# Optimization experiments

Measured on AMD Instinct MI355X. Metric: run time of the kernel, lower is better.

Reference implementation:

```python
import jax, jax.numpy as jnp
import numpy as np
from jax import lax

# dims: B batch, C=d_model=256, IMG=128, P=4 patch, H=W=32, L=H*W=1024
# D=d_inner=512 (ssm_ratio 2.0), N=d_state=16, R=dt_rank=16, K=4 scan directions
B, C, IMG, P = 2, 256, 128, 4
H = W = IMG // P
L = H * W
D_INNER, N, R, K = 512, 16, 16, 4


def layernorm(x, g, b, eps=1e-5):
    mu = jnp.mean(x, axis=-1, keepdims=True)
    var = jnp.var(x, axis=-1, keepdims=True)
    return (x - mu) * lax.rsqrt(var + eps) * g + b


def setup_inputs() -> dict:
    key = jax.random.key(0)
    ks = jax.random.split(key, 12)
    f = lambda i, shape, s=0.02: jax.random.normal(ks[i], shape, jnp.float32) * s
    A_init = jnp.tile(jnp.arange(1, N + 1, dtype=jnp.float32)[None, None, :], (K, D_INNER, 1))
    return {
        "x": jax.random.normal(ks[0], (B, C, IMG, IMG), jnp.float32),
        "patch_w": f(1, (C, C, P, P)),
        "patch_b": jnp.zeros((C,), jnp.float32),
        "ln_g": jnp.ones((C,), jnp.float32),
        "ln_b": jnp.zeros((C,), jnp.float32),
        "in_w": f(2, (2 * D_INNER, C)),
        "conv_w": f(3, (D_INNER, 1, 3, 3)),
        "conv_b": jnp.zeros((D_INNER,), jnp.float32),
        "xproj_w": f(4, (K, R + 2 * N, D_INNER)),
        "dt_w": f(5, (K, D_INNER, R)),
        "dt_b": f(6, (K, D_INNER), 0.1),
        "A_log": jnp.log(A_init),
        "Ds": jnp.ones((K, D_INNER), jnp.float32),
        "on_g": jnp.ones((D_INNER,), jnp.float32),
        "on_b": jnp.zeros((D_INNER,), jnp.float32),
        "out_w": f(7, (C, D_INNER)),
        "head_w": f(8, (1, C)),
        "head_b": jnp.zeros((1,), jnp.float32),
    }


def _forward(x, patch_w, patch_b, ln_g, ln_b, in_w, conv_w, conv_b, xproj_w,
             dt_w, dt_b, A_log, Ds, on_g, on_b, out_w, head_w, head_b):
    dn = ("NCHW", "OIHW", "NCHW")
    # GRL is identity in forward. Patch embed conv, stride = patch.
    t = lax.conv_general_dilated(x, patch_w, (P, P), "VALID", dimension_numbers=dn)
    t = t + patch_b[None, :, None, None]
    t = jnp.transpose(t, (0, 2, 3, 1))                      # (B,H,W,C)

    # ---- VSS block: t + SS2D(LN(t)) ----
    u = layernorm(t, ln_g, ln_b)
    xz = jnp.einsum("bhwc,ec->bhwe", u, in_w)               # (B,H,W,2D)
    xc, z = jnp.split(xz, 2, axis=-1)
    xc = jnp.transpose(xc, (0, 3, 1, 2))                    # (B,D,H,W)
    xc = lax.conv_general_dilated(xc, conv_w, (1, 1), "SAME",
                                  dimension_numbers=dn, feature_group_count=D_INNER)
    xc = jax.nn.silu(xc + conv_b[None, :, None, None])

    # cross-scan: row-major, col-major, and their reverses -> (B,K,D,L)
    x_hw = xc.reshape(B, D_INNER, L)
    x_wh = jnp.transpose(xc, (0, 1, 3, 2)).reshape(B, D_INNER, L)
    xs = jnp.stack([x_hw, x_wh], axis=1)
    xs = jnp.concatenate([xs, jnp.flip(xs, axis=-1)], axis=1)  # (B,4,D,L)

    x_dbl = jnp.einsum("bkdl,kcd->bkcl", xs, xproj_w)          # (B,K,R+2N,L)
    dts_r = x_dbl[:, :, :R]
    Bs = x_dbl[:, :, R:R + N]                                  # (B,K,N,L)
    Cs = x_dbl[:, :, R + N:]                                   # (B,K,N,L)
    dts = jnp.einsum("bkrl,kdr->bkdl", dts_r, dt_w) + dt_b[None, :, :, None]
    dts = jax.nn.softplus(dts)                                 # (B,K,D,L)

    A = -jnp.exp(A_log)                                        # (K,D,N)
    dA = jnp.exp(dts[:, :, :, None, :] * A[None, :, :, :, None])      # (B,K,D,N,L)
    dBu = (dts * xs)[:, :, :, None, :] * Bs[:, :, None, :, :]         # (B,K,D,N,L)

    dA_t = jnp.moveaxis(dA, -1, 0)        # (L,B,K,D,N)
    dBu_t = jnp.moveaxis(dBu, -1, 0)
    Cs_t = jnp.moveaxis(Cs, -1, 0)        # (L,B,K,N)

    def step(h, inputs):
        dA_i, dBu_i, C_i = inputs
        h = dA_i * h + dBu_i
        y = jnp.einsum("bkdn,bkn->bkd", h, C_i)
        return h, y

    h0 = jnp.zeros((B, K, D_INNER, N), xs.dtype)
    _, ys = lax.scan(step, h0, (dA_t, dBu_t, Cs_t))           # ys: (L,B,K,D)
    ys = jnp.moveaxis(ys, 0, -1)                               # (B,K,D,L)
    ys = ys + Ds[None, :, :, None] * xs

    # cross-merge (invert the 4 scan orders and sum)
    y_rev = jnp.flip(ys[:, 2:], axis=-1)                        # (B,2,D,L)
    y_hw = ys[:, 0] + y_rev[:, 0]
    y_wh = ys[:, 1] + y_rev[:, 1]
    y_wh = jnp.transpose(y_wh.reshape(B, D_INNER, W, H), (0, 1, 3, 2)).reshape(B, D_INNER, L)
    y = (y_hw + y_wh).reshape(B, D_INNER, H, W)
    y = jnp.transpose(y, (0, 2, 3, 1))                          # (B,H,W,D)

    y = layernorm(y, on_g, on_b) * jax.nn.silu(z)
    ss_out = jnp.einsum("bhwd,cd->bhwc", y, out_w)
    t = t + ss_out

    # global average pool + head
    pooled = jnp.mean(t, axis=(1, 2))                           # (B,C)
    return pooled @ head_w.T + head_b


def reference(x, patch_w, patch_b, ln_g, ln_b, in_w, conv_w, conv_b, xproj_w,
              dt_w, dt_b, A_log, Ds, on_g, on_b, out_w, head_w, head_b):
    return _forward(x, patch_w, patch_b, ln_g, ln_b, in_w, conv_w, conv_b, xproj_w,
                    dt_w, dt_b, A_log, Ds, on_g, on_b, out_w, head_w, head_b)
```

## Files before the change

### kernel.cpp

```cpp
#include <hip/hip_runtime.h>
#include <math.h>


typedef __attribute__((ext_vector_type(4))) float f32x4;
typedef __attribute__((ext_vector_type(8))) short bf16x8;

__device__ __forceinline__ ushort bf16_rn(float f) {
  uint u = __float_as_uint(f);
  return (ushort)((u + 0x7fffu + ((u >> 16) & 1u)) >> 16);
}
__device__ __forceinline__ float bf2f(uint us) { return __uint_as_float(us << 16); }
__device__ __forceinline__ uint packbf(float a, float b) {
  return (uint)bf16_rn(a) | ((uint)bf16_rn(b) << 16);
}

__global__ __launch_bounds__(256) void split_all(
    const float* __restrict__ pw, const float* __restrict__ iw,
    const float* __restrict__ ow, const float* __restrict__ xw,
    ushort* __restrict__ pwh, ushort* __restrict__ pwl,
    ushort* __restrict__ iwh, ushort* __restrict__ iwl,
    ushort* __restrict__ owh, ushort* __restrict__ owl,
    ushort* __restrict__ xwh, ushort* __restrict__ xwl) {
  int i = blockIdx.x * 256 + threadIdx.x;
  const float* src; ushort* hi; ushort* lo; int off;
  if (i < 1048576)      { src = pw; hi = pwh; lo = pwl; off = i; }
  else if (i < 1310720) { src = iw; hi = iwh; lo = iwl; off = i - 1048576; }
  else if (i < 1441792) { src = ow; hi = owh; lo = owl; off = i - 1310720; }
  else if (i < 1540096) { src = xw; hi = xwh; lo = xwl; off = i - 1441792; }
  else return;
  float f = src[off];
  ushort h = bf16_rn(f);
  hi[off] = h;
  lo[off] = bf16_rn(f - __uint_as_float(((uint)h) << 16));
}

__global__ __launch_bounds__(256) void im2col_bf16(const float* __restrict__ x,
    ushort* __restrict__ Ap) {
  __shared__ __align__(16) ushort tile[32][136];
  int c0 = blockIdx.x * 8, hh = blockIdx.y, b = blockIdx.z;
  int tid = threadIdx.x;
  int ci = tid >> 5, ph = (tid >> 3) & 3, w4 = tid & 7;
  const float* src = x + (((long)(b * 256 + c0 + ci) * 128 + 4 * hh + ph) * 128 + 16 * w4);
  #pragma unroll
  for (int j = 0; j < 4; ++j) {
    float4 v = *(const float4*)(src + 4 * j);
    uint2 pk;
    pk.x = packbf(v.x, v.y);
    pk.y = packbf(v.z, v.w);
    *(uint2*)&tile[w4 * 4 + j][ci * 16 + ph * 4] = pk;
  }
  __syncthreads();
  int w = tid >> 3;
  long rowbase = ((long)(b * 1024 + hh * 32 + w)) * 4096 + c0 * 16;
  #pragma unroll
  for (int i = 0; i < 2; ++i) {
    int gr = (tid & 7) + 8 * i;
    *(uint4*)&Ap[rowbase + gr * 8] = *(const uint4*)&tile[w][gr * 8];
  }
}

__global__ __launch_bounds__(512) void mfma_bf(
    const ushort* __restrict__ A, const ushort* __restrict__ Bhi,
    const ushort* __restrict__ Blo, float* __restrict__ Cout, float* __restrict__ C2,
    int M, int N, int K, int kchunk, int mode)
{
  __shared__ __align__(16) ushort Ah[128 * 64];
  __shared__ __align__(16) ushort Bh[64 * 64];
  __shared__ __align__(16) ushort Bl[64 * 64];
  int tid = threadIdx.x;
  int n0 = blockIdx.x * 64;
  int m0 = blockIdx.y * 128;
  int k0 = blockIdx.z * kchunk;
  int wid = tid >> 6, lane = tid & 63;
  int wm = wid >> 1, wn = wid & 1;
  int lrow = lane & 15, g = lane >> 4;
  f32x4 acc[2][2] = {};
  int nkt = kchunk >> 6;
  for (int kt = 0; kt < nkt; ++kt) {
    int kb = k0 + (kt << 6);
    {
      int gi = tid & 7;
      #pragma unroll
      for (int i = 0; i < 2; ++i) {
        int row = (tid >> 3) + (i << 6);
        uint4 v = *(const uint4*)&A[(long)(m0 + row) * K + kb + gi * 8];
        *(uint4*)&Ah[row * 64 + ((gi ^ (row & 7)) << 3)] = v;
      }
      int row = tid >> 3;
      long off = (long)(n0 + row) * K + kb + gi * 8;
      int la = row * 64 + ((gi ^ (row & 7)) << 3);
      *(uint4*)&Bh[la] = *(const uint4*)&Bhi[off];
      *(uint4*)&Bl[la] = *(const uint4*)&Blo[off];
    }
    __syncthreads();
    #pragma unroll
    for (int kk = 0; kk < 2; ++kk) {
      bf16x8 af[2], bhf[2], blf[2];
      #pragma unroll
      for (int mi = 0; mi < 2; ++mi) {
        int row = wm * 32 + mi * 16 + lrow;
        af[mi] = *(const bf16x8*)&Ah[row * 64 + ((((kk << 2) + g) ^ (row & 7)) << 3)];
      }
      #pragma unroll
      for (int ni = 0; ni < 2; ++ni) {
        int row = wn * 32 + ni * 16 + lrow;
        int col = (((kk << 2) + g) ^ (row & 7)) << 3;
        bhf[ni] = *(const bf16x8*)&Bh[row * 64 + col];
        blf[ni] = *(const bf16x8*)&Bl[row * 64 + col];
      }
      #pragma unroll
      for (int mi = 0; mi < 2; ++mi)
        #pragma unroll
        for (int ni = 0; ni < 2; ++ni) {
          acc[mi][ni] = __builtin_amdgcn_mfma_f32_16x16x32_bf16(af[mi], bhf[ni], acc[mi][ni], 0, 0, 0);
          acc[mi][ni] = __builtin_amdgcn_mfma_f32_16x16x32_bf16(af[mi], blf[ni], acc[mi][ni], 0, 0, 0);
        }
    }
    __syncthreads();
  }
  int r4 = lane >> 4;
  if (mode == 2) {
    bool xhalf = (n0 < 512);
    #pragma unroll
    for (int mi = 0; mi < 2; ++mi)
      #pragma unroll
      for (int ni = 0; ni < 2; ++ni) {
        int n = n0 + wn * 32 + ni * 16 + lrow;
        int mb = m0 + wm * 32 + mi * 16 + r4 * 4;
        int bb = mb >> 10, l = mb & 1023;
        if (xhalf) {
          float4 o = make_float4(acc[mi][ni][0], acc[mi][ni][1], acc[mi][ni][2], acc[mi][ni][3]);
          *(float4*)(Cout + ((long)(bb * 512 + n)) * 1024 + l) = o;
        } else {
          #pragma unroll
          for (int r = 0; r < 4; ++r)
            C2[(long)(mb + r) * 512 + (n - 512)] = acc[mi][ni][r];
        }
      }
  } else {
    long zoff = (long)blockIdx.z * M * N;
    #pragma unroll
    for (int mi = 0; mi < 2; ++mi)
      #pragma unroll
      for (int ni = 0; ni < 2; ++ni) {
        int n = n0 + wn * 32 + ni * 16 + lrow;
        int mb = m0 + wm * 32 + mi * 16 + r4 * 4;
        #pragma unroll
        for (int r = 0; r < 4; ++r)
          Cout[zoff + (long)(mb + r) * N + n] = acc[mi][ni][r];
      }
  }
}

__global__ __launch_bounds__(256) void mfma_x(
    const ushort* __restrict__ A, const ushort* __restrict__ Bhi,
    const ushort* __restrict__ Blo, float* __restrict__ xdbl)
{
  __shared__ __align__(16) ushort Ah[64 * 64];
  __shared__ __align__(16) ushort Bh[48 * 64];
  __shared__ __align__(16) ushort Bl[48 * 64];
  int tid = threadIdx.x;
  int m0 = blockIdx.x * 64;
  int z = blockIdx.y, k = z & 3;
  const ushort* Az = A + (long)z * 524288;
  const ushort* Bhz = Bhi + (long)k * 24576;
  const ushort* Blz = Blo + (long)k * 24576;
  int lane = tid & 63, wv = tid >> 6;
  int lrow = lane & 15, g = lane >> 4;
  f32x4 acc[3] = {};
  for (int kt = 0; kt < 8; ++kt) {
    int kb = kt << 6;
    #pragma unroll
    for (int i = 0; i < 2; ++i) {
      int idx = i * 256 + tid;
      int row = idx >> 3, gi = idx & 7;
      uint4 v = *(const uint4*)&Az[(long)(m0 + row) * 512 + kb + gi * 8];
      *(uint4*)&Ah[row * 64 + ((gi ^ (row & 7)) << 3)] = v;
      if (idx < 384) {
        long off = (long)row * 512 + kb + gi * 8;
        int la = row * 64 + ((gi ^ (row & 7)) << 3);
        *(uint4*)&Bh[la] = *(const uint4*)&Bhz[off];
        *(uint4*)&Bl[la] = *(const uint4*)&Blz[off];
      }
    }
    __syncthreads();
    #pragma unroll
    for (int kk = 0; kk < 2; ++kk) {
      int arow = wv * 16 + lrow;
      bf16x8 af = *(const bf16x8*)&Ah[arow * 64 + ((((kk << 2) + g) ^ (arow & 7)) << 3)];
      #pragma unroll
      for (int ni = 0; ni < 3; ++ni) {
        int brow = ni * 16 + lrow;
        int col = (((kk << 2) + g) ^ (brow & 7)) << 3;
        bf16x8 bh = *(const bf16x8*)&Bh[brow * 64 + col];
        bf16x8 bl = *(const bf16x8*)&Bl[brow * 64 + col];
        acc[ni] = __builtin_amdgcn_mfma_f32_16x16x32_bf16(af, bh, acc[ni], 0, 0, 0);
        acc[ni] = __builtin_amdgcn_mfma_f32_16x16x32_bf16(af, bl, acc[ni], 0, 0, 0);
      }
    }
    __syncthreads();
  }
  float* Cz = xdbl + (long)z * 49152;
  int r4 = lane >> 4;
  #pragma unroll
  for (int ni = 0; ni < 3; ++ni) {
    int n = ni * 16 + lrow;
    int mb = m0 + wv * 16 + r4 * 4;
    #pragma unroll
    for (int r = 0; r < 4; ++r)
      Cz[(long)(mb + r) * 48 + n] = acc[ni][r];
  }
}

__global__ __launch_bounds__(256) void reduce_split(const float* __restrict__ P,
    float* __restrict__ C, const float* __restrict__ bias,
    int MN, int N, int S, int accumulate) {
  int i = blockIdx.x * 256 + threadIdx.x;
  if (i * 4 >= MN) return;
  float4 v = make_float4(0.f, 0.f, 0.f, 0.f);
  for (int s = 0; s < S; ++s) {
    float4 p = *(const float4*)(P + (long)s * MN + i * 4);
    v.x += p.x; v.y += p.y; v.z += p.z; v.w += p.w;
  }
  if (bias) {
    float4 bv = *(const float4*)(bias + ((i * 4) & (N - 1)));
    v.x += bv.x; v.y += bv.y; v.z += bv.z; v.w += bv.w;
  }
  if (accumulate) {
    float4 o = *(const float4*)(C + (long)i * 4);
    v.x += o.x; v.y += o.y; v.z += o.z; v.w += o.w;
  }
  *(float4*)(C + (long)i * 4) = v;
}

__device__ __forceinline__ float blk_sum(float v, float* sm) {
  #pragma unroll
  for (int o = 32; o > 0; o >>= 1) v += __shfl_down(v, o);
  int wid = threadIdx.x >> 6, lane = threadIdx.x & 63;
  __syncthreads();
  if (lane == 0) sm[wid] = v;
  __syncthreads();
  int nw = blockDim.x >> 6;
  float r = 0.f;
  for (int i = 0; i < nw; ++i) r += sm[i];
  return r;
}

__global__ __launch_bounds__(256) void reduce_ln1(const float* __restrict__ P,
    float* __restrict__ t, const float* __restrict__ bias,
    const float* __restrict__ g, const float* __restrict__ b,
    ushort* __restrict__ u) {
  __shared__ float sm[8];
  int m = blockIdx.x, c = threadIdx.x;
  float v = bias[c];
  #pragma unroll
  for (int s = 0; s < 8; ++s) v += P[(long)s * 524288 + m * 256 + c];
  t[(long)m * 256 + c] = v;
  float s1 = blk_sum(v, sm);
  float s2 = blk_sum(v * v, sm);
  float mu = s1 * (1.f / 256.f);
  float var = s2 * (1.f / 256.f) - mu * mu;
  float rs = rsqrtf(var + 1e-5f);
  u[(long)m * 256 + c] = bf16_rn((v - mu) * rs * g[c] + b[c]);
}

template<int ACT>
__global__ __launch_bounds__(256) void gemm_nt(
    const float* __restrict__ Ag, const float* __restrict__ Bg,
    const float* __restrict__ biasg, float* Cg,
    int M, int N, int Kd, int lda, int ldb, int ldc,
    long sA, long sB, long sBias, long sC, int bmod, int accumulate)
{
  __shared__ __align__(16) float As[64 * 36];
  __shared__ float Bs[32 * 33];
  int z = blockIdx.z;
  int zb = (bmod > 1) ? (z % bmod) : 0;
  const float* A = Ag + (long)z * sA;
  const float* Bm = Bg + (long)zb * sB;
  const float* bias = biasg ? (biasg + (long)zb * sBias) : nullptr;
  float* C = Cg + (long)z * sC;
  int tid = threadIdx.x;
  int n0 = blockIdx.x * 32;
  int m0 = blockIdx.y * 64;
  int tn = tid & 7, tm = tid >> 3;
  float acc[2][4] = {};
  int nk = (Kd + 31) >> 5;
  for (int kt = 0; kt < nk; ++kt) {
    int k0 = kt << 5;
    #pragma unroll
    for (int i = 0; i < 2; ++i) {
      int idx = i * 256 + tid;
      int row = idx >> 3, c4 = idx & 7;
      int m = m0 + row, k = k0 + c4 * 4;
      float4 v = make_float4(0.f, 0.f, 0.f, 0.f);
      if (m < M && k < Kd) v = *(const float4*)(A + (long)m * lda + k);
      *(float4*)&As[row * 36 + c4 * 4] = v;
    }
    {
      int row = tid >> 3, c4 = tid & 7;
      int n = n0 + row, k = k0 + c4 * 4;
      float4 v = make_float4(0.f, 0.f, 0.f, 0.f);
      if (n < N && k < Kd) v = *(const float4*)(Bm + (long)n * ldb + k);
      Bs[row * 33 + c4 * 4 + 0] = v.x;
      Bs[row * 33 + c4 * 4 + 1] = v.y;
      Bs[row * 33 + c4 * 4 + 2] = v.z;
      Bs[row * 33 + c4 * 4 + 3] = v.w;
    }
    __syncthreads();
    #pragma unroll
    for (int kk = 0; kk < 32; ++kk) {
      float a0 = As[(tm * 2 + 0) * 36 + kk];
      float a1 = As[(tm * 2 + 1) * 36 + kk];
      #pragma unroll
      for (int j = 0; j < 4; ++j) {
        float bv = Bs[(tn * 4 + j) * 33 + kk];
        acc[0][j] += a0 * bv;
        acc[1][j] += a1 * bv;
      }
    }
    __syncthreads();
  }
  bool fullN = (n0 + 32 <= N);
  #pragma unroll
  for (int i = 0; i < 2; ++i) {
    int m = m0 + tm * 2 + i;
    if (m >= M) continue;
    float r[4];
    #pragma unroll
    for (int j = 0; j < 4; ++j) {
      int n = n0 + tn * 4 + j;
      float v = acc[i][j];
      if (bias && n < N) v += bias[n];
      if (ACT == 1) v = (v > 20.f) ? v : __logf(1.f + __expf(v));
      r[j] = v;
    }
    long base = (long)m * ldc + n0 + tn * 4;
    if (fullN) {
      float4 o = make_float4(r[0], r[1], r[2], r[3]);
      if (accumulate) {
        float4 old = *(float4*)(C + base);
        o.x += old.x; o.y += old.y; o.z += old.z; o.w += old.w;
      }
      *(float4*)(C + base) = o;
    } else {
      #pragma unroll
      for (int j = 0; j < 4; ++j) {
        int n = n0 + tn * 4 + j;
        if (n < N) {
          float v = r[j];
          if (accumulate) v += C[(long)m * ldc + n];
          C[(long)m * ldc + n] = v;
        }
      }
    }
  }
}

__global__ __launch_bounds__(256) void dwconv_kernel(const float* __restrict__ xc,
    const float* __restrict__ cw, const float* __restrict__ cb, ushort* __restrict__ out) {
  __shared__ float plane[32][33];
  int d = blockIdx.x, b = blockIdx.y;
  long base = ((long)b * 512 + d) * 1024;
  int tid = threadIdx.x;
  float4 v = *(const float4*)(xc + base + tid * 4);
  int h0 = (tid * 4) >> 5, w0 = (tid * 4) & 31;
  plane[h0][w0 + 0] = v.x; plane[h0][w0 + 1] = v.y;
  plane[h0][w0 + 2] = v.z; plane[h0][w0 + 3] = v.w;
  float w9[9];
  #pragma unroll
  for (int i = 0; i < 9; ++i) w9[i] = cw[d * 9 + i];
  float bias = cb[d];
  __syncthreads();
  float o4[4];
  #pragma unroll
  for (int j = 0; j < 4; ++j) {
    int p = tid * 4 + j, h = p >> 5, w = p & 31;
    float acc = 0.f;
    #pragma unroll
    for (int dh = -1; dh <= 1; ++dh) {
      int hy = h + dh;
      if (hy < 0 || hy > 31) continue;
      #pragma unroll
      for (int dw = -1; dw <= 1; ++dw) {
        int wx = w + dw;
        if (wx < 0 || wx > 31) continue;
        acc += w9[(dh + 1) * 3 + (dw + 1)] * plane[hy][wx];
      }
    }
    acc += bias;
    o4[j] = acc / (1.f + __expf(-acc));
  }
  uint2 o2;
  o2.x = packbf(o4[0], o4[1]);
  o2.y = packbf(o4[2], o4[3]);
  *(uint2*)&out[base + tid * 4] = o2;
}

__global__ __launch_bounds__(256) void build_xsT(const ushort* __restrict__ xca,
    ushort* __restrict__ xsTb) {
  __shared__ ushort tile[32][34];
  int h = blockIdx.x;
  int d0 = blockIdx.y * 32;
  int z = blockIdx.z;
  int b = z >> 2, k = z & 3;
  int tid = threadIdx.x;
  int a = tid >> 5, q = tid & 31;
  #pragma unroll
  for (int i = 0; i < 4; ++i) {
    int di = a + i * 8;
    tile[di][q] = xca[((long)(b * 512 + d0 + di)) * 1024 + h * 32 + q];
  }
  __syncthreads();
  #pragma unroll
  for (int i = 0; i < 4; ++i) {
    int w = a + i * 8;
    int r;
    if (k == 0) r = h * 32 + w;
    else if (k == 1) r = w * 32 + h;
    else if (k == 2) r = 1023 - (h * 32 + w);
    else r = 1023 - (w * 32 + h);
    xsTb[((long)z * 1024 + r) * 512 + d0 + q] = tile[q][w];
  }
}

template<bool FINAL>
__global__ __launch_bounds__(128) void scan_chunk5(
    const float* __restrict__ dts, ushort* xsb, const float* __restrict__ xdbl,
    const float* __restrict__ A_log, const float* __restrict__ Ds,
    float* __restrict__ Pb, float* __restrict__ hpb)
{
  __shared__ float sdt[16][64], sxv[16][64], sy[16][64];
  __shared__ float sBC[32][32];
  int tid = threadIdx.x;
  int dl = tid >> 1, ng = tid & 1;
  int d0 = blockIdx.x * 64;
  int d = d0 + dl;
  int c = blockIdx.y;
  int z = blockIdx.z;
  int k = z & 3;
  long baseD = (long)z * 524288;
  int l0 = c * 32;
  float a[8], h[8];
  #pragma unroll
  for (int j = 0; j < 8; ++j) {
    a[j] = -__expf(A_log[((long)k * 512 + d) * 16 + ng * 8 + j]);
    h[j] = 0.f;
  }
  int gbase = c * 65536 + z * 8192 + d * 16 + ng * 8;
  float Dv = 0.f;
  if (FINAL) {
    #pragma unroll
    for (int j = 0; j < 8; ++j) h[j] = hpb[gbase + j];
    Dv = Ds[k * 512 + d];
  }
  #pragma unroll
  for (int i = 0; i < 2; ++i) {
    int idx = i * 128 + tid;
    int l = idx >> 3, q = idx & 7;
    *(float4*)&sBC[l][q * 4] =
        *(const float4*)(xdbl + (long)z * 49152 + (long)(l0 + l) * 48 + 16 + q * 4);
  }
  int sli = tid >> 4;
  int sdj = (tid & 15) * 4;
  int xli = tid >> 3;
  int xdj = (tid & 7) * 8;
  float4 rdt[2]; uint4 rxv;
  #pragma unroll
  for (int i = 0; i < 2; ++i)
    rdt[i] = *(const float4*)(dts + baseD + (long)(l0 + sli + i * 8) * 512 + d0 + sdj);
  rxv = *(const uint4*)&xsb[baseD + (long)(l0 + xli) * 512 + d0 + xdj];
  float dtsum = 0.f;
  for (int t = 0; t < 2; ++t) {
    #pragma unroll
    for (int i = 0; i < 2; ++i)
      *(float4*)&sdt[sli + i * 8][sdj] = rdt[i];
    {
      float4 f0, f1;
      f0.x = bf2f(rxv.x & 0xffff); f0.y = bf2f(rxv.x >> 16);
      f0.z = bf2f(rxv.y & 0xffff); f0.w = bf2f(rxv.y >> 16);
      f1.x = bf2f(rxv.z & 0xffff); f1.y = bf2f(rxv.z >> 16);
      f1.z = bf2f(rxv.w & 0xffff); f1.w = bf2f(rxv.w >> 16);
      *(float4*)&sxv[xli][xdj] = f0;
      *(float4*)&sxv[xli][xdj + 4] = f1;
    }
    __syncthreads();
    if (t == 0) {
      #pragma unroll
      for (int i = 0; i < 2; ++i)
        rdt[i] = *(const float4*)(dts + baseD + (long)(l0 + 16 + sli + i * 8) * 512 + d0 + sdj);
      rxv = *(const uint4*)&xsb[baseD + (long)(l0 + 16 + xli) * 512 + d0 + xdj];
    }
    #pragma unroll
    for (int li = 0; li < 16; ++li) {
      float dt = sdt[li][dl];
      float xv = sxv[li][dl];
      float w = dt * xv;
      int lr = t * 16 + li;
      float4 B0 = *(const float4*)&sBC[lr][ng * 8];
      float4 B1 = *(const float4*)&sBC[lr][ng * 8 + 4];
      if (!FINAL) {
        dtsum += dt;
        h[0] = __expf(dt * a[0]) * h[0] + w * B0.x;
        h[1] = __expf(dt * a[1]) * h[1] + w * B0.y;
        h[2] = __expf(dt * a[2]) * h[2] + w * B0.z;
        h[3] = __expf(dt * a[3]) * h[3] + w * B0.w;
        h[4] = __expf(dt * a[4]) * h[4] + w * B1.x;
        h[5] = __expf(dt * a[5]) * h[5] + w * B1.y;
        h[6] = __expf(dt * a[6]) * h[6] + w * B1.z;
        h[7] = __expf(dt * a[7]) * h[7] + w * B1.w;
      } else {
        float4 C0 = *(const float4*)&sBC[lr][16 + ng * 8];
        float4 C1 = *(const float4*)&sBC[lr][16 + ng * 8 + 4];
        float p;
        h[0] = __expf(dt * a[0]) * h[0] + w * B0.x; p  = h[0] * C0.x;
        h[1] = __expf(dt * a[1]) * h[1] + w * B0.y; p += h[1] * C0.y;
        h[2] = __expf(dt * a[2]) * h[2] + w * B0.z; p += h[2] * C0.z;
        h[3] = __expf(dt * a[3]) * h[3] + w * B0.w; p += h[3] * C0.w;
        h[4] = __expf(dt * a[4]) * h[4] + w * B1.x; p += h[4] * C1.x;
        h[5] = __expf(dt * a[5]) * h[5] + w * B1.y; p += h[5] * C1.y;
        h[6] = __expf(dt * a[6]) * h[6] + w * B1.z; p += h[6] * C1.z;
        h[7] = __expf(dt * a[7]) * h[7] + w * B1.w; p += h[7] * C1.w;
        p += __shfl_xor(p, 1);
        if (ng == 0) sy[li][dl] = p + Dv * xv;
      }
    }
    __syncthreads();
    if (FINAL) {
      float4 f0 = *(float4*)&sy[xli][xdj];
      float4 f1 = *(float4*)&sy[xli][xdj + 4];
      uint4 o;
      o.x = packbf(f0.x, f0.y); o.y = packbf(f0.z, f0.w);
      o.z = packbf(f1.x, f1.y); o.w = packbf(f1.z, f1.w);
      *(uint4*)&xsb[baseD + (long)(l0 + t * 16 + xli) * 512 + d0 + xdj] = o;
    }
  }
  if (!FINAL) {
    float4 pv;
    #pragma unroll
    for (int i = 0; i < 2; ++i) {
      pv.x = __expf(dtsum * a[i * 4 + 0]);
      pv.y = __expf(dtsum * a[i * 4 + 1]);
      pv.z = __expf(dtsum * a[i * 4 + 2]);
      pv.w = __expf(dtsum * a[i * 4 + 3]);
      *(float4*)(Pb + gbase + i * 4) = pv;
      *(float4*)(hpb + gbase + i * 4) = make_float4(h[i*4+0], h[i*4+1], h[i*4+2], h[i*4+3]);
    }
  }
}

__global__ __launch_bounds__(256) void scan_prefix(const float* __restrict__ Pb,
    float* __restrict__ hpb) {
  int g = blockIdx.x * 256 + threadIdx.x;
  float h = 0.f;
  #pragma unroll
  for (int c = 0; c < 32; ++c) {
    float P = Pb[c * 65536 + g];
    float hp = hpb[c * 65536 + g];
    hpb[c * 65536 + g] = h;
    h = P * h + hp;
  }
}

__global__ __launch_bounds__(256) void combine_ln2gate(const ushort* __restrict__ ys,
    const float* __restrict__ zb, ushort* __restrict__ out,
    const float* __restrict__ g, const float* __restrict__ b) {
  __shared__ float sm[8];
  int m = blockIdx.x, tid = threadIdx.x;
  int bb = m >> 10, l = m & 1023;
  int hh = l >> 5, w = l & 31;
  int lw = w * 32 + hh;
  long b4 = (long)bb * 4;
  uint u0 = *(const uint*)&ys[((b4 + 0) * 1024 + l) * 512 + tid * 2];
  uint u1 = *(const uint*)&ys[((b4 + 2) * 1024 + (1023 - l)) * 512 + tid * 2];
  uint u2 = *(const uint*)&ys[((b4 + 1) * 1024 + lw) * 512 + tid * 2];
  uint u3 = *(const uint*)&ys[((b4 + 3) * 1024 + (1023 - lw)) * 512 + tid * 2];
  float v0 = bf2f(u0 & 0xffff) + bf2f(u1 & 0xffff) + bf2f(u2 & 0xffff) + bf2f(u3 & 0xffff);
  float v1 = bf2f(u0 >> 16) + bf2f(u1 >> 16) + bf2f(u2 >> 16) + bf2f(u3 >> 16);
  float s1 = blk_sum(v0 + v1, sm);
  float s2 = blk_sum(v0 * v0 + v1 * v1, sm);
  float mu = s1 * (1.f / 512.f);
  float var = s2 * (1.f / 512.f) - mu * mu;
  float rs = rsqrtf(var + 1e-5f);
  float2 gg = *(const float2*)(g + tid * 2);
  float2 bbv = *(const float2*)(b + tid * 2);
  float2 zz = *(const float2*)(zb + (long)m * 512 + tid * 2);
  float y0 = ((v0 - mu) * rs * gg.x + bbv.x) * (zz.x / (1.f + __expf(-zz.x)));
  float y1 = ((v1 - mu) * rs * gg.y + bbv.y) * (zz.y / (1.f + __expf(-zz.y)));
  *(uint*)&out[(long)m * 512 + tid * 2] = packbf(y0, y1);
}

__global__ __launch_bounds__(256) void head_partial(const float* __restrict__ t,
    const float* __restrict__ hw, float* __restrict__ part) {
  __shared__ float sm[8];
  int j = blockIdx.x, b = blockIdx.y;
  int c = threadIdx.x;
  float s = 0.f;
  for (int l = j * 64; l < j * 64 + 64; ++l) s += t[((long)b * 1024 + l) * 256 + c];
  s *= hw[c];
  float tot = blk_sum(s, sm);
  if (c == 0) part[b * 16 + j] = tot;
}

__global__ void head_final(const float* __restrict__ part, const float* __restrict__ hb, float* __restrict__ out) {
  int tid = threadIdx.x;
  float v = (tid < 32) ? part[tid] : 0.f;
  #pragma unroll
  for (int o = 1; o < 16; o <<= 1) v += __shfl_xor(v, o);
  if (tid < 32 && (tid & 15) == 0) out[tid >> 4] = v * (1.f / 1024.f) + hb[0];
}

extern "C" void kernel_launch(void* const* d_in, const int* in_sizes, int n_in,
                              void* d_out, int out_size, void* d_ws, size_t ws_size,
                              hipStream_t stream) {
  const float* x       = (const float*)d_in[0];
  const float* patch_w = (const float*)d_in[1];
  const float* patch_b = (const float*)d_in[2];
  const float* ln_g    = (const float*)d_in[3];
  const float* ln_b    = (const float*)d_in[4];
  const float* in_w    = (const float*)d_in[5];
  const float* conv_w  = (const float*)d_in[6];
  const float* conv_b  = (const float*)d_in[7];
  const float* xproj_w = (const float*)d_in[8];
  const float* dt_w    = (const float*)d_in[9];
  const float* dt_b    = (const float*)d_in[10];
  const float* A_log   = (const float*)d_in[11];
  const float* Ds      = (const float*)d_in[12];
  const float* on_g    = (const float*)d_in[13];
  const float* on_b    = (const float*)d_in[14];
  const float* out_w   = (const float*)d_in[15];
  const float* head_w  = (const float*)d_in[16];
  const float* head_b  = (const float*)d_in[17];

  float* ws = (float*)d_ws;
  float* t_buf   = ws;
  float* u_buf   = t_buf + 524288;
  float* xz_buf  = u_buf + 524288;
  float* xc_buf  = xz_buf + 2097152;
  float* xca_buf = xc_buf + 1048576;
  float* xsT_buf = xca_buf + 1048576;
  float* xdbl_buf= xsT_buf + 4194304;
  float* dts_buf = xdbl_buf + 393216;
  float* part_buf= dts_buf + 4194304;
  float* tail    = part_buf + 32;
  ushort* A_p    = (ushort*)xsT_buf;
  ushort* pw_hi  = (ushort*)xz_buf;
  ushort* pw_lo  = (ushort*)(xz_buf + 524288);
  float*  z_buf  = xz_buf;
  float*  P_patch= dts_buf;
  float*  P_out  = dts_buf;
  ushort* u_bf   = (ushort*)u_buf;
  ushort* xca_bf = (ushort*)xca_buf;
  ushort* y_bf   = (ushort*)xca_buf;
  ushort* iw_hi  = (ushort*)tail;
  ushort* iw_lo  = (ushort*)(tail + 131072);
  ushort* ow_hi  = (ushort*)(tail + 262144);
  ushort* ow_lo  = (ushort*)(tail + 327680);
  ushort* xw_hi  = (ushort*)(tail + 393216);
  ushort* xw_lo  = (ushort*)(tail + 442368);
  ushort* xsT_bf = (ushort*)(tail + 491520);
  float*  P_buf  = tail + 2588672;
  float*  hp_buf = tail + 4685824;

  split_all<<<6017, 256, 0, stream>>>(patch_w, in_w, out_w, xproj_w,
      pw_hi, pw_lo, iw_hi, iw_lo, ow_hi, ow_lo, xw_hi, xw_lo);
  im2col_bf16<<<dim3(32, 32, 2), 256, 0, stream>>>(x, A_p);
  mfma_bf<<<dim3(4, 16, 8), 512, 0, stream>>>(A_p, pw_hi, pw_lo, P_patch, nullptr,
      2048, 256, 4096, 512, 0);
  reduce_ln1<<<2048, 256, 0, stream>>>(P_patch, t_buf, patch_b, ln_g, ln_b, u_bf);
  mfma_bf<<<dim3(16, 16, 1), 512, 0, stream>>>(u_bf, iw_hi, iw_lo, xc_buf, z_buf,
      2048, 1024, 256, 256, 2);
  dwconv_kernel<<<dim3(512, 2), 256, 0, stream>>>(xc_buf, conv_w, conv_b, xca_bf);
  build_xsT<<<dim3(32, 16, 8), 256, 0, stream>>>(xca_bf, xsT_bf);
  mfma_x<<<dim3(16, 8), 256, 0, stream>>>(xsT_bf, xw_hi, xw_lo, xdbl_buf);
  gemm_nt<1><<<dim3(16, 16, 8), 256, 0, stream>>>(xdbl_buf, dt_w, dt_b, dts_buf,
      1024, 512, 16, 48, 16, 512, 49152, 8192, 512, 524288, 4, 0);
  scan_chunk5<false><<<dim3(8, 32, 8), 128, 0, stream>>>(dts_buf, xsT_bf, xdbl_buf,
      A_log, Ds, P_buf, hp_buf);
  scan_prefix<<<256, 256, 0, stream>>>(P_buf, hp_buf);
  scan_chunk5<true><<<dim3(8, 32, 8), 128, 0, stream>>>(dts_buf, xsT_bf, xdbl_buf,
      A_log, Ds, nullptr, hp_buf);
  combine_ln2gate<<<2048, 256, 0, stream>>>(xsT_bf, z_buf, y_bf, on_g, on_b);
  mfma_bf<<<dim3(4, 16, 4), 512, 0, stream>>>(y_bf, ow_hi, ow_lo, P_out, nullptr,
      2048, 256, 512, 128, 0);
  reduce_split<<<512, 256, 0, stream>>>(P_out, t_buf, nullptr, 524288, 256, 4, 1);
  head_partial<<<dim3(16, 2), 256, 0, stream>>>(t_buf, head_w, part_buf);
  head_final<<<1, 64, 0, stream>>>(part_buf, head_b, (float*)d_out);
}
```

Measured before the change: 148.3 us.

## Fuse dt projection and softplus into scan kernels; store xc as bf16

Removes the separate gemm_nt launch that computed dt = softplus(xdbl[:, :16] @ dt_w^T + dt_b) into a large fp32 buffer. Both scan passes now recompute dt in shared memory from the 16-wide dt_rank slice, so the multi-megabyte dts write and its two reads go away. The in_proj GEMM also writes the conv input half as bf16 instead of fp32, halving that tensor's traffic into the depthwise conv. The costs are dt computed twice (once per scan pass), larger shared memory per block, and extra rounding of xc to bf16 before the conv.

```diff
diff --git a/kernel.cpp b/kernel.cpp
--- a/kernel.cpp
+++ b/kernel.cpp
@@ -121,6 +121,7 @@
   int r4 = lane >> 4;
   if (mode == 2) {
     bool xhalf = (n0 < 512);
+    ushort* xcb = (ushort*)Cout;
     #pragma unroll
     for (int mi = 0; mi < 2; ++mi)
       #pragma unroll
@@ -129,8 +130,10 @@
         int mb = m0 + wm * 32 + mi * 16 + r4 * 4;
         int bb = mb >> 10, l = mb & 1023;
         if (xhalf) {
-          float4 o = make_float4(acc[mi][ni][0], acc[mi][ni][1], acc[mi][ni][2], acc[mi][ni][3]);
-          *(float4*)(Cout + ((long)(bb * 512 + n)) * 1024 + l) = o;
+          uint2 o;
+          o.x = packbf(acc[mi][ni][0], acc[mi][ni][1]);
+          o.y = packbf(acc[mi][ni][2], acc[mi][ni][3]);
+          *(uint2*)&xcb[((long)(bb * 512 + n)) * 1024 + l] = o;
         } else {
           #pragma unroll
           for (int r = 0; r < 4; ++r)
@@ -264,108 +267,16 @@
   u[(long)m * 256 + c] = bf16_rn((v - mu) * rs * g[c] + b[c]);
 }
 
-template<int ACT>
-__global__ __launch_bounds__(256) void gemm_nt(
-    const float* __restrict__ Ag, const float* __restrict__ Bg,
-    const float* __restrict__ biasg, float* Cg,
-    int M, int N, int Kd, int lda, int ldb, int ldc,
-    long sA, long sB, long sBias, long sC, int bmod, int accumulate)
-{
-  __shared__ __align__(16) float As[64 * 36];
-  __shared__ float Bs[32 * 33];
-  int z = blockIdx.z;
-  int zb = (bmod > 1) ? (z % bmod) : 0;
-  const float* A = Ag + (long)z * sA;
-  const float* Bm = Bg + (long)zb * sB;
-  const float* bias = biasg ? (biasg + (long)zb * sBias) : nullptr;
-  float* C = Cg + (long)z * sC;
-  int tid = threadIdx.x;
-  int n0 = blockIdx.x * 32;
-  int m0 = blockIdx.y * 64;
-  int tn = tid & 7, tm = tid >> 3;
-  float acc[2][4] = {};
-  int nk = (Kd + 31) >> 5;
-  for (int kt = 0; kt < nk; ++kt) {
-    int k0 = kt << 5;
-    #pragma unroll
-    for (int i = 0; i < 2; ++i) {
-      int idx = i * 256 + tid;
-      int row = idx >> 3, c4 = idx & 7;
-      int m = m0 + row, k = k0 + c4 * 4;
-      float4 v = make_float4(0.f, 0.f, 0.f, 0.f);
-      if (m < M && k < Kd) v = *(const float4*)(A + (long)m * lda + k);
-      *(float4*)&As[row * 36 + c4 * 4] = v;
-    }
-    {
-      int row = tid >> 3, c4 = tid & 7;
-      int n = n0 + row, k = k0 + c4 * 4;
-      float4 v = make_float4(0.f, 0.f, 0.f, 0.f);
-      if (n < N && k < Kd) v = *(const float4*)(Bm + (long)n * ldb + k);
-      Bs[row * 33 + c4 * 4 + 0] = v.x;
-      Bs[row * 33 + c4 * 4 + 1] = v.y;
-      Bs[row * 33 + c4 * 4 + 2] = v.z;
-      Bs[row * 33 + c4 * 4 + 3] = v.w;
-    }
-    __syncthreads();
-    #pragma unroll
-    for (int kk = 0; kk < 32; ++kk) {
-      float a0 = As[(tm * 2 + 0) * 36 + kk];
-      float a1 = As[(tm * 2 + 1) * 36 + kk];
-      #pragma unroll
-      for (int j = 0; j < 4; ++j) {
-        float bv = Bs[(tn * 4 + j) * 33 + kk];
-        acc[0][j] += a0 * bv;
-        acc[1][j] += a1 * bv;
-      }
-    }
-    __syncthreads();
-  }
-  bool fullN = (n0 + 32 <= N);
-  #pragma unroll
-  for (int i = 0; i < 2; ++i) {
-    int m = m0 + tm * 2 + i;
-    if (m >= M) continue;
-    float r[4];
-    #pragma unroll
-    for (int j = 0; j < 4; ++j) {
-      int n = n0 + tn * 4 + j;
-      float v = acc[i][j];
-      if (bias && n < N) v += bias[n];
-      if (ACT == 1) v = (v > 20.f) ? v : __logf(1.f + __expf(v));
-      r[j] = v;
-    }
-    long base = (long)m * ldc + n0 + tn * 4;
-    if (fullN) {
-      float4 o = make_float4(r[0], r[1], r[2], r[3]);
-      if (accumulate) {
-        float4 old = *(float4*)(C + base);
-        o.x += old.x; o.y += old.y; o.z += old.z; o.w += old.w;
-      }
-      *(float4*)(C + base) = o;
-    } else {
-      #pragma unroll
-      for (int j = 0; j < 4; ++j) {
-        int n = n0 + tn * 4 + j;
-        if (n < N) {
-          float v = r[j];
-          if (accumulate) v += C[(long)m * ldc + n];
-          C[(long)m * ldc + n] = v;
-        }
-      }
-    }
-  }
-}
-
-__global__ __launch_bounds__(256) void dwconv_kernel(const float* __restrict__ xc,
+__global__ __launch_bounds__(256) void dwconv_kernel(const ushort* __restrict__ xc,
     const float* __restrict__ cw, const float* __restrict__ cb, ushort* __restrict__ out) {
   __shared__ float plane[32][33];
   int d = blockIdx.x, b = blockIdx.y;
   long base = ((long)b * 512 + d) * 1024;
   int tid = threadIdx.x;
-  float4 v = *(const float4*)(xc + base + tid * 4);
+  uint2 v = *(const uint2*)&xc[base + tid * 4];
   int h0 = (tid * 4) >> 5, w0 = (tid * 4) & 31;
-  plane[h0][w0 + 0] = v.x; plane[h0][w0 + 1] = v.y;
-  plane[h0][w0 + 2] = v.z; plane[h0][w0 + 3] = v.w;
+  plane[h0][w0 + 0] = bf2f(v.x & 0xffff); plane[h0][w0 + 1] = bf2f(v.x >> 16);
+  plane[h0][w0 + 2] = bf2f(v.y & 0xffff); plane[h0][w0 + 3] = bf2f(v.y >> 16);
   float w9[9];
   #pragma unroll
   for (int i = 0; i < 9; ++i) w9[i] = cw[d * 9 + i];
@@ -424,13 +335,17 @@
 }
 
 template<bool FINAL>
-__global__ __launch_bounds__(128) void scan_chunk5(
-    const float* __restrict__ dts, ushort* xsb, const float* __restrict__ xdbl,
+__global__ __launch_bounds__(128) void scan_chunk6(
+    const float* __restrict__ xdbl, ushort* xsb,
+    const float* __restrict__ dtw, const float* __restrict__ dtb,
     const float* __restrict__ A_log, const float* __restrict__ Ds,
     float* __restrict__ Pb, float* __restrict__ hpb)
 {
-  __shared__ float sdt[16][64], sxv[16][64], sy[16][64];
+  __shared__ float sdt[32][64];
+  __shared__ float sxv[16][64];
+  __shared__ float sy[16][64];
   __shared__ float sBC[32][32];
+  float (*sR)[16] = (float(*)[16])sy;
   int tid = threadIdx.x;
   int dl = tid >> 1, ng = tid & 1;
   int d0 = blockIdx.x * 64;
@@ -440,12 +355,28 @@
   int k = z & 3;
   long baseD = (long)z * 524288;
   int l0 = c * 32;
+  const float* xdz = xdbl + (long)z * 49152 + (long)l0 * 48;
+  #pragma unroll
+  for (int i = 0; i < 2; ++i) {
+    int idx = i * 128 + tid;
+    int l = idx >> 3, q = idx & 7;
+    *(float4*)&sBC[l][q * 4] = *(const float4*)(xdz + l * 48 + 16 + q * 4);
+  }
+  {
+    int l = tid >> 2, q = tid & 3;
+    *(float4*)&sR[l][q * 4] = *(const float4*)(xdz + l * 48 + q * 4);
+  }
   float a[8], h[8];
   #pragma unroll
   for (int j = 0; j < 8; ++j) {
     a[j] = -__expf(A_log[((long)k * 512 + d) * 16 + ng * 8 + j]);
     h[j] = 0.f;
   }
+  float4 wr0 = *(const float4*)(dtw + ((long)k * 512 + d) * 16);
+  float4 wr1 = *(const float4*)(dtw + ((long)k * 512 + d) * 16 + 4);
+  float4 wr2 = *(const float4*)(dtw + ((long)k * 512 + d) * 16 + 8);
+  float4 wr3 = *(const float4*)(dtw + ((long)k * 512 + d) * 16 + 12);
+  float dbias = dtb[k * 512 + d];
   int gbase = c * 65536 + z * 8192 + d * 16 + ng * 8;
   float Dv = 0.f;
   if (FINAL) {
@@ -453,27 +384,24 @@
     for (int j = 0; j < 8; ++j) h[j] = hpb[gbase + j];
     Dv = Ds[k * 512 + d];
   }
-  #pragma unroll
-  for (int i = 0; i < 2; ++i) {
-    int idx = i * 128 + tid;
-    int l = idx >> 3, q = idx & 7;
-    *(float4*)&sBC[l][q * 4] =
-        *(const float4*)(xdbl + (long)z * 49152 + (long)(l0 + l) * 48 + 16 + q * 4);
-  }
-  int sli = tid >> 4;
-  int sdj = (tid & 15) * 4;
+  __syncthreads();
+  #pragma unroll
+  for (int li = 0; li < 16; ++li) {
+    int l = ng * 16 + li;
+    const float* rr = &sR[l][0];
+    float acc = dbias;
+    acc += wr0.x * rr[0];  acc += wr0.y * rr[1];  acc += wr0.z * rr[2];  acc += wr0.w * rr[3];
+    acc += wr1.x * rr[4];  acc += wr1.y * rr[5];  acc += wr1.z * rr[6];  acc += wr1.w * rr[7];
+    acc += wr2.x * rr[8];  acc += wr2.y * rr[9];  acc += wr2.z * rr[10]; acc += wr2.w * rr[11];
+    acc += wr3.x * rr[12]; acc += wr3.y * rr[13]; acc += wr3.z * rr[14]; acc += wr3.w * rr[15];
+    sdt[l][dl] = (acc > 20.f) ? acc : __logf(1.f + __expf(acc));
+  }
+  __syncthreads();
   int xli = tid >> 3;
   int xdj = (tid & 7) * 8;
-  float4 rdt[2]; uint4 rxv;
-  #pragma unroll
-  for (int i = 0; i < 2; ++i)
-    rdt[i] = *(const float4*)(dts + baseD + (long)(l0 + sli + i * 8) * 512 + d0 + sdj);
-  rxv = *(const uint4*)&xsb[baseD + (long)(l0 + xli) * 512 + d0 + xdj];
+  uint4 rxv = *(const uint4*)&xsb[baseD + (long)(l0 + xli) * 512 + d0 + xdj];
   float dtsum = 0.f;
   for (int t = 0; t < 2; ++t) {
-    #pragma unroll
-    for (int i = 0; i < 2; ++i)
-      *(float4*)&sdt[sli + i * 8][sdj] = rdt[i];
     {
       float4 f0, f1;
       f0.x = bf2f(rxv.x & 0xffff); f0.y = bf2f(rxv.x >> 16);
@@ -484,18 +412,14 @@
       *(float4*)&sxv[xli][xdj + 4] = f1;
     }
     __syncthreads();
-    if (t == 0) {
-      #pragma unroll
-      for (int i = 0; i < 2; ++i)
-        rdt[i] = *(const float4*)(dts + baseD + (long)(l0 + 16 + sli + i * 8) * 512 + d0 + sdj);
+    if (t == 0)
       rxv = *(const uint4*)&xsb[baseD + (long)(l0 + 16 + xli) * 512 + d0 + xdj];
-    }
     #pragma unroll
     for (int li = 0; li < 16; ++li) {
-      float dt = sdt[li][dl];
+      int lr = t * 16 + li;
+      float dt = sdt[lr][dl];
       float xv = sxv[li][dl];
       float w = dt * xv;
-      int lr = t * 16 + li;
       float4 B0 = *(const float4*)&sBC[lr][ng * 8];
       float4 B1 = *(const float4*)&sBC[lr][ng * 8 + 4];
       if (!FINAL) {
@@ -639,16 +563,17 @@
   float* xca_buf = xc_buf + 1048576;
   float* xsT_buf = xca_buf + 1048576;
   float* xdbl_buf= xsT_buf + 4194304;
-  float* dts_buf = xdbl_buf + 393216;
-  float* part_buf= dts_buf + 4194304;
+  float* spl_buf = xdbl_buf + 393216;
+  float* part_buf= spl_buf + 4194304;
   float* tail    = part_buf + 32;
   ushort* A_p    = (ushort*)xsT_buf;
   ushort* pw_hi  = (ushort*)xz_buf;
   ushort* pw_lo  = (ushort*)(xz_buf + 524288);
   float*  z_buf  = xz_buf;
-  float*  P_patch= dts_buf;
-  float*  P_out  = dts_buf;
+  float*  P_patch= spl_buf;
+  float*  P_out  = spl_buf;
   ushort* u_bf   = (ushort*)u_buf;
+  ushort* xc_bf  = (ushort*)xc_buf;
   ushort* xca_bf = (ushort*)xca_buf;
   ushort* y_bf   = (ushort*)xca_buf;
   ushort* iw_hi  = (ushort*)tail;
@@ -669,16 +594,14 @@
   reduce_ln1<<<2048, 256, 0, stream>>>(P_patch, t_buf, patch_b, ln_g, ln_b, u_bf);
   mfma_bf<<<dim3(16, 16, 1), 512, 0, stream>>>(u_bf, iw_hi, iw_lo, xc_buf, z_buf,
       2048, 1024, 256, 256, 2);
-  dwconv_kernel<<<dim3(512, 2), 256, 0, stream>>>(xc_buf, conv_w, conv_b, xca_bf);
+  dwconv_kernel<<<dim3(512, 2), 256, 0, stream>>>(xc_bf, conv_w, conv_b, xca_bf);
   build_xsT<<<dim3(32, 16, 8), 256, 0, stream>>>(xca_bf, xsT_bf);
   mfma_x<<<dim3(16, 8), 256, 0, stream>>>(xsT_bf, xw_hi, xw_lo, xdbl_buf);
-  gemm_nt<1><<<dim3(16, 16, 8), 256, 0, stream>>>(xdbl_buf, dt_w, dt_b, dts_buf,
-      1024, 512, 16, 48, 16, 512, 49152, 8192, 512, 524288, 4, 0);
-  scan_chunk5<false><<<dim3(8, 32, 8), 128, 0, stream>>>(dts_buf, xsT_bf, xdbl_buf,
-      A_log, Ds, P_buf, hp_buf);
+  scan_chunk6<false><<<dim3(8, 32, 8), 128, 0, stream>>>(xdbl_buf, xsT_bf,
+      dt_w, dt_b, A_log, Ds, P_buf, hp_buf);
   scan_prefix<<<256, 256, 0, stream>>>(P_buf, hp_buf);
-  scan_chunk5<true><<<dim3(8, 32, 8), 128, 0, stream>>>(dts_buf, xsT_bf, xdbl_buf,
-      A_log, Ds, nullptr, hp_buf);
+  scan_chunk6<true><<<dim3(8, 32, 8), 128, 0, stream>>>(xdbl_buf, xsT_bf,
+      dt_w, dt_b, A_log, Ds, nullptr, hp_buf);
   combine_ln2gate<<<2048, 256, 0, stream>>>(xsT_bf, z_buf, y_bf, on_g, on_b);
   mfma_bf<<<dim3(4, 16, 4), 512, 0, stream>>>(y_bf, ow_hi, ow_lo, P_out, nullptr,
       2048, 256, 512, 128, 0);
```

After: 140.8 us. 5.1% less time.
